# Performance work log

Measured on AMD Instinct MI355X. Metric: run time of the kernel, lower is better.

Reference implementation:

```python
import jax, jax.numpy as jnp
import numpy as np

STRIDE = 16
H = 100
W = 100
C = 1024
A = 9  # anchors per location
IOU_THRESH = 0.7
MIN_SIZE = 16.0


def _conv2d(x, w, b):
    # x: [N,C,H,W], w: [O,I,kh,kw] (torch OIHW), 'same' padding, stride 1
    y = jax.lax.conv_general_dilated(
        x, w, window_strides=(1, 1), padding='SAME',
        dimension_numbers=('NCHW', 'OIHW', 'NCHW'))
    return y + b[None, :, None, None]


def _nms_keep(boxes, valid, iou_thresh):
    # boxes: [N,4] (y1,x1,y2,x2) sorted by descending score; valid: [N] bool
    n = boxes.shape[0]
    y1, x1, y2, x2 = boxes[:, 0], boxes[:, 1], boxes[:, 2], boxes[:, 3]
    areas = (y2 - y1) * (x2 - x1)
    idx = jnp.arange(n)

    def body(i, keep):
        iy1 = jnp.maximum(y1[i], y1)
        ix1 = jnp.maximum(x1[i], x1)
        iy2 = jnp.minimum(y2[i], y2)
        ix2 = jnp.minimum(x2[i], x2)
        inter = jnp.maximum(iy2 - iy1, 0.0) * jnp.maximum(ix2 - ix1, 0.0)
        iou = inter / (areas[i] + areas - inter + 1e-8)
        suppress = (iou > iou_thresh) & (idx > i)
        return jnp.where(keep[i], keep & ~suppress, keep)

    return jax.lax.fori_loop(0, n, body, valid)


def _make_anchor_map():
    ratios = np.array([0.5, 1.0, 2.0])
    sizes = np.array([128.0, 256.0, 512.0])
    ah = (sizes[:, None] * np.sqrt(ratios)[None, :]).reshape(-1)  # [9]
    aw = (sizes[:, None] / np.sqrt(ratios)[None, :]).reshape(-1)  # [9]
    cy = (np.arange(H) + 0.5) * STRIDE
    cx = (np.arange(W) + 0.5) * STRIDE
    am = np.zeros((H, W, A, 4), dtype=np.float32)
    am[..., 0] = cy[:, None, None]
    am[..., 1] = cx[None, :, None]
    am[..., 2] = ah[None, None, :]
    am[..., 3] = aw[None, None, :]
    return jnp.asarray(am.reshape(H, W, A * 4))


def setup_inputs() -> dict:
    key = jax.random.key(0)
    ks = jax.random.split(key, 4)
    feature_map = jax.random.normal(ks[0], (1, C, H, W), jnp.float32)
    # module init: normal(0, 0.01) weights, zero biases
    w1 = jax.random.normal(ks[1], (C, C, 3, 3), jnp.float32) * 0.01
    b1 = jnp.zeros((C,), jnp.float32)
    w_cls = jax.random.normal(ks[2], (A, C, 1, 1), jnp.float32) * 0.01
    b_cls = jnp.zeros((A,), jnp.float32)
    w_box = jax.random.normal(ks[3], (A * 4, C, 1, 1), jnp.float32) * 0.01
    b_box = jnp.zeros((A * 4,), jnp.float32)
    return {
        'feature_map': feature_map,
        'image_shape': jnp.array([3, H * STRIDE, W * STRIDE], jnp.int32),
        'anchor_map': _make_anchor_map(),
        'anchor_valid_map': jnp.ones((H, W, A), jnp.int32),
        'max_proposals_pre_nms': 6000,
        'max_proposals_post_nms': 300,
        'w1': w1, 'b1': b1,
        'w_cls': w_cls, 'b_cls': b_cls,
        'w_box': w_box, 'b_box': b_box,
    }


def reference(feature_map, image_shape, anchor_map, anchor_valid_map,
              max_proposals_pre_nms, max_proposals_post_nms,
              w1, b1, w_cls, b_cls, w_box, b_box):
    pre = int(max_proposals_pre_nms)
    post = int(max_proposals_post_nms)

    y = jax.nn.relu(_conv2d(feature_map, w1, b1))
    objectness_score_map = jax.nn.sigmoid(_conv2d(y, w_cls, b_cls))  # [1,9,H,W]
    box_deltas_map = _conv2d(y, w_box, b_box)                        # [1,36,H,W]
    # NCHW -> NHWC, like permute(0,2,3,1)
    objectness_score_map = jnp.transpose(objectness_score_map, (0, 2, 3, 1))
    box_deltas_map = jnp.transpose(box_deltas_map, (0, 2, 3, 1))

    h, w, a = anchor_valid_map.shape
    n = h * w * a
    anchors = anchor_map.reshape(n, 4)                # (cy, cx, ah, aw)
    scores = objectness_score_map.reshape(n)
    deltas = jax.lax.stop_gradient(box_deltas_map.reshape(n, 4))  # .detach()
    # allow_edge_proposals=True -> no valid filtering

    # decode (means=0, stds=1): center = c + t*s, size = s*exp(t)
    center = anchors[:, 0:2] + deltas[:, 0:2] * anchors[:, 2:4]
    size = anchors[:, 2:4] * jnp.exp(deltas[:, 2:4])
    proposals = jnp.concatenate([center - 0.5 * size, center + 0.5 * size], axis=1)

    # argsort ascending then flip == descending (matches torch code)
    order = jnp.argsort(scores)[::-1][:pre]
    proposals = proposals[order]
    scores_sorted = scores[order]

    # clip to image
    y1x1 = jnp.maximum(proposals[:, 0:2], 0.0)
    y2 = jnp.minimum(proposals[:, 2], image_shape[1].astype(proposals.dtype))
    x2 = jnp.minimum(proposals[:, 3], image_shape[2].astype(proposals.dtype))
    proposals = jnp.concatenate([y1x1, y2[:, None], x2[:, None]], axis=1)

    height = proposals[:, 2] - proposals[:, 0]
    width = proposals[:, 3] - proposals[:, 1]
    valid = (height >= MIN_SIZE) & (width >= MIN_SIZE)

    keep = _nms_keep(proposals, valid, IOU_THRESH)

    # fixed-shape selection of first `post` kept boxes (score-ordered)
    pos = jnp.where(keep, jnp.arange(pre), pre)
    pos = jnp.sort(pos)[:post]
    ok = pos < pre
    safe = jnp.minimum(pos, pre - 1)
    out_proposals = jnp.where(ok[:, None], proposals[safe], 0.0)  # [post,4]

    return objectness_score_map, box_deltas_map, out_proposals
```

## Files before the change

### kernel.cpp

```cpp
#include <hip/hip_runtime.h>
#include <hip/hip_fp16.h>
#include <stdint.h>

#define HH 100
#define WW 100
#define NPIX 10000
#define CIN 1024
#define COUT 1024
#define NA 9
#define NANCH 90000
#define PRE 6000
#define POST 300
#define SORTN 131072
#define MASKW 96
#define NW 94
#define K9 9216
#define SPAD 10404
#define WSCALE 1024.0f
#define KH 48

#define PXT 160
#define ABYTES 8192
#define BBYTES 10240
#define BUFB 36864
#define NSTEP 288

typedef unsigned short u16;
typedef _Float16 f16x8 __attribute__((ext_vector_type(8)));
typedef float f32x4 __attribute__((ext_vector_type(4)));

__device__ __forceinline__ void gload16(const u16* g, char* l)
{
    __builtin_amdgcn_global_load_lds((const void*)g, (void*)l, 16, 0, 0);
}

__global__ __launch_bounds__(256) void xsplit(
    const float* __restrict__ x, u16* __restrict__ xt1, u16* __restrict__ xt2)
{
    __shared__ unsigned sh[32][257];
    const int t = threadIdx.x;
    const int px0 = blockIdx.x * 32;
    const int ci0 = blockIdx.y * 256;
    for (int it = 0; it < 32; ++it) {
        int idx = it * 256 + t;
        int a = idx >> 5, b = idx & 31;
        int p = px0 + b;
        float v = (p < NPIX) ? x[(size_t)(ci0 + a) * NPIX + p] : 0.f;
        __half h1 = __float2half_rn(v);
        __half h2 = __float2half_rn(v - __half2float(h1));
        sh[b][a] = ((unsigned)__half_as_ushort(h1) << 16) | __half_as_ushort(h2);
    }
    __syncthreads();
    for (int it = 0; it < 8; ++it) {
        int u = it * 256 + t;
        int pl = u >> 6, cq = u & 63;
        int p = px0 + pl;
        if (p >= NPIX) continue;
        int r = p / 100, c = p - r * 100;
        int spx = (r + 1) * 102 + (c + 1);
        unsigned w0 = sh[pl][cq * 4 + 0], w1 = sh[pl][cq * 4 + 1];
        unsigned w2 = sh[pl][cq * 4 + 2], w3 = sh[pl][cq * 4 + 3];
        ushort4 v1 = make_ushort4((u16)(w0 >> 16), (u16)(w1 >> 16), (u16)(w2 >> 16), (u16)(w3 >> 16));
        ushort4 v2 = make_ushort4((u16)(w0 & 0xffff), (u16)(w1 & 0xffff), (u16)(w2 & 0xffff), (u16)(w3 & 0xffff));
        size_t o = (size_t)spx * 1024 + ci0 + cq * 4;
        *(ushort4*)&xt1[o] = v1;
        *(ushort4*)&xt2[o] = v2;
    }
}

__global__ __launch_bounds__(256) void xborder(u16* __restrict__ xt1, u16* __restrict__ xt2)
{
    const int idx = blockIdx.x;
    int spx;
    if (idx < 102) spx = idx;
    else if (idx < 204) spx = 10302 + (idx - 102);
    else { int k = idx - 204; spx = (1 + (k >> 1)) * 102 + (k & 1) * 101; }
    const int t = threadIdx.x;
    size_t o = (size_t)spx * 1024 + t * 4;
    *(ushort4*)&xt1[o] = make_ushort4(0, 0, 0, 0);
    *(ushort4*)&xt2[o] = make_ushort4(0, 0, 0, 0);
}

__global__ __launch_bounds__(256) void wsplit(
    const float* __restrict__ w1, u16* __restrict__ wp1, u16* __restrict__ wp2)
{
    __shared__ float sw[K9];
    const int t = threadIdx.x;
    const int co = blockIdx.x;
    for (int it = 0; it < 36; ++it)
        sw[it * 256 + t] = w1[(size_t)co * K9 + it * 256 + t];
    __syncthreads();
    for (int tap = 0; tap < 9; ++tap) {
        for (int it = 0; it < 4; ++it) {
            int ci = it * 256 + t;
            float v = sw[ci * 9 + tap] * WSCALE;
            __half h1 = __float2half_rn(v);
            __half h2 = __float2half_rn(v - __half2float(h1));
            size_t o = (size_t)tap * (COUT * 1024) + (size_t)co * 1024 + ci;
            wp1[o] = __half_as_ushort(h1);
            wp2[o] = __half_as_ushort(h2);
        }
    }
}

__global__ __launch_bounds__(256, 2) void conv_mfma(
    const u16* __restrict__ xt1, const u16* __restrict__ xt2,
    const u16* __restrict__ wp1, const u16* __restrict__ wp2,
    const float* __restrict__ b1, float* __restrict__ y)
{
    __shared__ __align__(16) char lds[2 * BUFB];
    const int t = threadIdx.x;
    const int co0 = blockIdx.x * 128;
    const int px0 = blockIdx.y * PXT;
    const int lane = t & 63;
    const int wv = __builtin_amdgcn_readfirstlane(t >> 6);
    const int wm = (wv >> 1) * 64;
    const int wn = (wv & 1) * 80;

    const int qs = (lane & 3) ^ ((lane >> 3) & 3);
    const int aln = (lane >> 2) * 1024 + qs * 8;

    const int ar0 = wv * 32, ar1 = wv * 32 + 16;
    const size_t aOff0 = (size_t)(co0 + ar0) * 1024 + aln;
    const size_t aOff1 = (size_t)(co0 + ar1) * 1024 + aln;

    const int nb = (wv < 2) ? 3 : 2;
    size_t bOff[3]; int bLds[3];
#pragma unroll
    for (int s = 0; s < 3; ++s) {
        int r0 = (wv + 4 * s) * 16;
        if (r0 >= PXT) r0 = 0;
        int p = px0 + r0 + (lane >> 2);
        if (p > NPIX - 1) p = NPIX - 1;
        int rr = p / 100, cc = p - rr * 100;
        bOff[s] = (size_t)((rr + 1) * 102 + cc + 1) * 1024 + qs * 8;
        bLds[s] = r0 * 64;
    }

    const int qf = ((lane >> 4) ^ (((lane & 15) >> 1) & 3)) * 16;
    const int fA = (wm + (lane & 15)) * 64 + qf;
    const int fB = 16384 + (wn + (lane & 15)) * 64 + qf;

    f32x4 acc[4][5] = {};

    auto STAGE = [&](int buf, int tap, int ci0) {
        const int dy = (tap * 11) >> 5;
        const int tsh = (dy - 1) * 102 + (tap - dy * 3) - 1;
        const size_t adelta = (size_t)tap * 1048576 + ci0;
        const ptrdiff_t bdelta = (ptrdiff_t)tsh * 1024 + ci0;
        char* lb = lds + buf * BUFB;
        gload16(wp1 + aOff0 + adelta, lb + ar0 * 64);
        gload16(wp1 + aOff1 + adelta, lb + ar1 * 64);
        gload16(wp2 + aOff0 + adelta, lb + ABYTES + ar0 * 64);
        gload16(wp2 + aOff1 + adelta, lb + ABYTES + ar1 * 64);
#pragma unroll
        for (int s = 0; s < 3; ++s) {
            if (s < nb) {
                gload16(xt1 + (ptrdiff_t)bOff[s] + bdelta, lb + 16384 + bLds[s]);
                gload16(xt2 + (ptrdiff_t)bOff[s] + bdelta, lb + 26624 + bLds[s]);
            }
        }
    };

    auto COMPUTE = [&](int buf) {
        const char* lb = lds + buf * BUFB;
        f16x8 A1[4], A2[4], B1[5], B2[5];
#pragma unroll
        for (int mi = 0; mi < 4; ++mi) {
            A1[mi] = *(const f16x8*)(lb + fA + mi * 1024);
            A2[mi] = *(const f16x8*)(lb + ABYTES + fA + mi * 1024);
        }
#pragma unroll
        for (int ni = 0; ni < 5; ++ni) {
            B1[ni] = *(const f16x8*)(lb + fB + ni * 1024);
            B2[ni] = *(const f16x8*)(lb + BBYTES + fB + ni * 1024);
        }
#pragma unroll
        for (int mi = 0; mi < 4; ++mi)
#pragma unroll
            for (int ni = 0; ni < 5; ++ni) {
                acc[mi][ni] = __builtin_amdgcn_mfma_f32_16x16x32_f16(A1[mi], B1[ni], acc[mi][ni], 0, 0, 0);
                acc[mi][ni] = __builtin_amdgcn_mfma_f32_16x16x32_f16(A1[mi], B2[ni], acc[mi][ni], 0, 0, 0);
                acc[mi][ni] = __builtin_amdgcn_mfma_f32_16x16x32_f16(A2[mi], B1[ni], acc[mi][ni], 0, 0, 0);
            }
    };

    STAGE(0, 0, 0);
    __syncthreads();
    for (int kk = 0; kk < NSTEP - 1; ++kk) {
        const int kn = kk + 1;
        STAGE(kn & 1, kn >> 5, (kn & 31) << 5);
        COMPUTE(kk & 1);
        __syncthreads();
    }
    COMPUTE((NSTEP - 1) & 1);

    const int q4 = (lane >> 4) * 4, nl = lane & 15;
    const float inv = 1.0f / WSCALE;
#pragma unroll
    for (int mi = 0; mi < 4; ++mi) {
        const int cob = co0 + wm + mi * 16 + q4;
        const float bb0 = b1[cob + 0], bb1 = b1[cob + 1];
        const float bb2 = b1[cob + 2], bb3 = b1[cob + 3];
#pragma unroll
        for (int ni = 0; ni < 5; ++ni) {
            const int px = px0 + wn + ni * 16 + nl;
            if (px < NPIX) {
                y[(size_t)(cob + 0) * NPIX + px] = fmaxf(acc[mi][ni][0] * inv + bb0, 0.f);
                y[(size_t)(cob + 1) * NPIX + px] = fmaxf(acc[mi][ni][1] * inv + bb1, 0.f);
                y[(size_t)(cob + 2) * NPIX + px] = fmaxf(acc[mi][ni][2] * inv + bb2, 0.f);
                y[(size_t)(cob + 3) * NPIX + px] = fmaxf(acc[mi][ni][3] * inv + bb3, 0.f);
            }
        }
    }
}

__global__ __launch_bounds__(256) void wh_prep(
    const float* __restrict__ wcls, const float* __restrict__ wbox,
    float* __restrict__ wh)
{
    int e = blockIdx.x * 256 + threadIdx.x;
    if (e >= CIN * KH) return;
    int c = e / KH, k = e - c * KH;
    float v = 0.f;
    if (k < 9) v = wcls[k * CIN + c];
    else if (k < 45) v = wbox[(k - 9) * CIN + c];
    wh[e] = v;
}

__global__ __launch_bounds__(256) void rpn_head(
    const float* __restrict__ y, const float* __restrict__ wh,
    const float* __restrict__ bcls, const float* __restrict__ bbox,
    const float* __restrict__ am, const int* __restrict__ ishape,
    float* __restrict__ out_scores, float* __restrict__ out_deltas,
    float4* __restrict__ boxes, unsigned long long* __restrict__ keys)
{
    __shared__ float red[4][64][KH + 1];
    const int t = threadIdx.x;
    const int lane = t & 63;
    const int q = __builtin_amdgcn_readfirstlane(t >> 6);
    const int p = blockIdx.x * 64 + lane;
    const int pp = (p < NPIX) ? p : (NPIX - 1);

    float acc[45];
#pragma unroll
    for (int k = 0; k < 45; ++k) acc[k] = 0.f;

    const float* __restrict__ yq  = y  + (size_t)q * 256 * NPIX + pp;
    const float* __restrict__ whq = wh + (size_t)q * 256 * KH;
    for (int c = 0; c < 256; ++c) {
        float yv = yq[(size_t)c * NPIX];
        const float* wr = whq + c * KH;
#pragma unroll
        for (int k = 0; k < 45; ++k) acc[k] += yv * wr[k];
    }

#pragma unroll
    for (int k = 0; k < 45; ++k) red[q][lane][k] = acc[k];
    __syncthreads();

    if (t >= 64 || p >= NPIX) return;

    float s[45];
#pragma unroll
    for (int k = 0; k < 45; ++k)
        s[k] = (red[0][lane][k] + red[1][lane][k]) + (red[2][lane][k] + red[3][lane][k]);

    const float imh = (float)ishape[1], imw = (float)ishape[2];
#pragma unroll
    for (int a = 0; a < 9; ++a) {
        const int i = p * NA + a;
        float logit = s[a] + bcls[a];
        float score = 1.f / (1.f + expf(-logit));
        float d0 = s[9 + a * 4 + 0] + bbox[a * 4 + 0];
        float d1 = s[9 + a * 4 + 1] + bbox[a * 4 + 1];
        float d2 = s[9 + a * 4 + 2] + bbox[a * 4 + 2];
        float d3 = s[9 + a * 4 + 3] + bbox[a * 4 + 3];
        out_scores[i] = score;
        out_deltas[i * 4 + 0] = d0;
        out_deltas[i * 4 + 1] = d1;
        out_deltas[i * 4 + 2] = d2;
        out_deltas[i * 4 + 3] = d3;

        float cy = am[i * 4 + 0], cx = am[i * 4 + 1];
        float ah = am[i * 4 + 2], aw = am[i * 4 + 3];
        float ctry = cy + d0 * ah, ctrx = cx + d1 * aw;
        float hh = ah * expf(d2), ww = aw * expf(d3);
        float y1 = fmaxf(ctry - 0.5f * hh, 0.f);
        float x1 = fmaxf(ctrx - 0.5f * ww, 0.f);
        float y2 = fminf(ctry + 0.5f * hh, imh);
        float x2 = fminf(ctrx + 0.5f * ww, imw);
        boxes[i] = make_float4(y1, x1, y2, x2);
        unsigned sb = __float_as_uint(score);
        keys[i] = ((unsigned long long)sb << 32) | (unsigned)i;
    }
}

__global__ __launch_bounds__(256) void key_pad(unsigned long long* __restrict__ keys)
{
    int i = NANCH + blockIdx.x * 256 + threadIdx.x;
    if (i < SORTN) keys[i] = 0ull;
}

__global__ __launch_bounds__(256) void bitonic_local(unsigned long long* keys)
{
    __shared__ unsigned long long s[2048];
    const int base = blockIdx.x * 2048, t = threadIdx.x;
    for (int k = t; k < 2048; k += 256) s[k] = keys[base + k];
    for (int L = 2; L <= 2048; L <<= 1) {
        for (int d = L >> 1; d >= 1; d >>= 1) {
            __syncthreads();
            for (int pr = t; pr < 1024; pr += 256) {
                int i = ((pr & ~(d - 1)) << 1) | (pr & (d - 1));
                int j = i + d;
                bool desc = (((base + i) & L) == 0);
                unsigned long long va = s[i], vb = s[j];
                bool sw = desc ? (va < vb) : (va > vb);
                if (sw) { s[i] = vb; s[j] = va; }
            }
        }
    }
    __syncthreads();
    for (int k = t; k < 2048; k += 256) keys[base + k] = s[k];
}

__global__ __launch_bounds__(256) void bitonic_gpass(unsigned long long* keys, int L, int d)
{
    int pr = blockIdx.x * 256 + threadIdx.x;
    int i = ((pr & ~(d - 1)) << 1) | (pr & (d - 1));
    int j = i + d;
    bool desc = ((i & L) == 0);
    unsigned long long va = keys[i], vb = keys[j];
    bool sw = desc ? (va < vb) : (va > vb);
    if (sw) { keys[i] = vb; keys[j] = va; }
}

__global__ __launch_bounds__(256) void bitonic_lmerge(unsigned long long* keys, int L)
{
    __shared__ unsigned long long s[2048];
    const int base = blockIdx.x * 2048, t = threadIdx.x;
    for (int k = t; k < 2048; k += 256) s[k] = keys[base + k];
    const bool desc = ((base & L) == 0);
    for (int d = 1024; d >= 1; d >>= 1) {
        __syncthreads();
        for (int pr = t; pr < 1024; pr += 256) {
            int i = ((pr & ~(d - 1)) << 1) | (pr & (d - 1));
            int j = i + d;
            unsigned long long va = s[i], vb = s[j];
            bool sw = desc ? (va < vb) : (va > vb);
            if (sw) { s[i] = vb; s[j] = va; }
        }
    }
    __syncthreads();
    for (int k = t; k < 2048; k += 256) keys[base + k] = s[k];
}

__global__ __launch_bounds__(256) void gather_sorted(
    const unsigned long long* __restrict__ keys, const float4* __restrict__ boxes,
    float4* __restrict__ box_s, unsigned long long* __restrict__ validw)
{
    int s = blockIdx.x * 256 + threadIdx.x;
    bool valid = false;
    if (s < PRE) {
        unsigned idx = (unsigned)(keys[s] & 0xffffffffull);
        float4 b = boxes[idx];
        box_s[s] = b;
        valid = ((b.z - b.x) >= 16.f) && ((b.w - b.y) >= 16.f);
    }
    unsigned long long bal = __ballot(valid);
    if ((threadIdx.x & 63) == 0) validw[s >> 6] = bal;
}

__global__ __launch_bounds__(128) void nms_mask(
    const float4* __restrict__ box_s, unsigned long long* __restrict__ mask)
{
    const int i = blockIdx.x;
    const int w = threadIdx.x;
    if (w >= NW) return;
    float4 bi = box_s[i];
    float areai = (bi.z - bi.x) * (bi.w - bi.y);
    unsigned long long m = 0ull;
    const int j0 = w * 64;
    if (j0 + 63 > i) {
#pragma unroll 4
        for (int b = 0; b < 64; ++b) {
            int j = j0 + b;
            if (j <= i || j >= PRE) continue;
            float4 bj = box_s[j];
            float areaj = (bj.z - bj.x) * (bj.w - bj.y);
            float iy1 = fmaxf(bi.x, bj.x), ix1 = fmaxf(bi.y, bj.y);
            float iy2 = fminf(bi.z, bj.z), ix2 = fminf(bi.w, bj.w);
            float inter = fmaxf(iy2 - iy1, 0.f) * fmaxf(ix2 - ix1, 0.f);
            float iou = inter / (areai + areaj - inter + 1e-8f);
            if (iou > 0.7f) m |= (1ull << b);
        }
    }
    mask[(size_t)i * MASKW + w] = m;
}

__global__ __launch_bounds__(64) void nms_scan(
    const unsigned long long* __restrict__ mask,
    const unsigned long long* __restrict__ validw,
    unsigned long long* __restrict__ keepw)
{
    const int l = threadIdx.x;
    unsigned long long r0 = ~validw[l];
    unsigned long long r1 = (l < NW - 64) ? ~validw[64 + l] : ~0ull;

    unsigned long long p0[16], p1[16];
#pragma unroll
    for (int k = 0; k < 16; ++k) {
        p0[k] = mask[(size_t)k * MASKW + l];
        p1[k] = (l < NW - 64) ? mask[(size_t)k * MASKW + 64 + l] : 0ull;
    }
    int kept = 0;
    for (int w = 0; w < NW && kept < POST; ++w) {
        unsigned long long Wc = (w < 64) ? __shfl(r0, w) : __shfl(r1, w - 64);
#pragma unroll 16
        for (int b = 0; b < 64; ++b) {
            int i = w * 64 + b;
            if (i >= PRE) break;
            int slot = i & 15;
            unsigned long long m0 = p0[slot], m1 = p1[slot];
            int nxt = i + 16;
            if (nxt < PRE) {
                p0[slot] = mask[(size_t)nxt * MASKW + l];
                p1[slot] = (l < NW - 64) ? mask[(size_t)nxt * MASKW + 64 + l] : 0ull;
            }
            if (!((Wc >> b) & 1ull)) {
                r0 |= m0; r1 |= m1;
                Wc = (w < 64) ? __shfl(r0, w) : __shfl(r1, w - 64);
                ++kept;
            }
        }
    }
    keepw[l] = ~r0;
    if (l < NW - 64) keepw[64 + l] = ~r1;
}

__global__ __launch_bounds__(256) void out_gather(
    const unsigned long long* __restrict__ keepw,
    const float4* __restrict__ box_s, float* __restrict__ outp)
{
    __shared__ unsigned long long kw_s[NW];
    __shared__ int prefix[NW];
    const int t = threadIdx.x;
    if (t < NW) kw_s[t] = keepw[t];
    __syncthreads();
    if (t == 0) {
        int cum = 0;
        for (int w = 0; w < NW; ++w) { prefix[w] = cum; cum += __popcll(kw_s[w]); }
    }
    for (int k = t; k < POST * 4; k += 256) outp[k] = 0.f;
    __syncthreads();
    for (int i = t; i < PRE; i += 256) {
        int w = i >> 6, b = i & 63;
        unsigned long long kw = kw_s[w];
        if ((kw >> b) & 1ull) {
            int rank = prefix[w] + __popcll(kw & ((1ull << b) - 1ull));
            if (rank < POST) {
                float4 bx = box_s[i];
                outp[rank * 4 + 0] = bx.x;
                outp[rank * 4 + 1] = bx.y;
                outp[rank * 4 + 2] = bx.z;
                outp[rank * 4 + 3] = bx.w;
            }
        }
    }
}

extern "C" void kernel_launch(void* const* d_in, const int* in_sizes, int n_in,
                              void* d_out, int out_size, void* d_ws, size_t ws_size,
                              hipStream_t stream)
{
    const float* x      = (const float*)d_in[0];
    const int*   ishape = (const int*)  d_in[1];
    const float* am     = (const float*)d_in[2];
    const float* w1   = (const float*)d_in[6];
    const float* b1   = (const float*)d_in[7];
    const float* wcls = (const float*)d_in[8];
    const float* bcls = (const float*)d_in[9];
    const float* wbox = (const float*)d_in[10];
    const float* bbox = (const float*)d_in[11];
    float* out = (float*)d_out;

    char* ws = (char*)d_ws;
    size_t off = 0;
    float* y  = (float*)(ws + off);  off += (size_t)COUT * NPIX * 4;
    u16* xt1  = (u16*)(ws + off);    off += (size_t)SPAD * 1024 * 2;
    u16* xt2  = (u16*)(ws + off);    off += (size_t)SPAD * 1024 * 2;
    u16* wp1  = (u16*)(ws + off);    off += (size_t)9 * COUT * 1024 * 2;
    u16* wp2  = (u16*)(ws + off);    off += (size_t)9 * COUT * 1024 * 2;
    float4* boxes = (float4*)(ws + off);              off += (size_t)NANCH * 16;
    unsigned long long* keys = (unsigned long long*)(ws + off); off += (size_t)SORTN * 8;
    float4* box_s = (float4*)(ws + off);              off += (size_t)PRE * 16;
    unsigned long long* validw = (unsigned long long*)(ws + off); off += 96 * 8;
    unsigned long long* keepw  = (unsigned long long*)(ws + off); off += 96 * 8;
    unsigned long long* maskb  = (unsigned long long*)(ws + off); off += (size_t)PRE * MASKW * 8;
    float* wh = (float*)(ws + off);  off += (size_t)CIN * KH * 4;

    xsplit<<<dim3(313, 4), 256, 0, stream>>>(x, xt1, xt2);
    xborder<<<404, 256, 0, stream>>>(xt1, xt2);
    wsplit<<<COUT, 256, 0, stream>>>(w1, wp1, wp2);
    wh_prep<<<(CIN * KH + 255) / 256, 256, 0, stream>>>(wcls, wbox, wh);
    conv_mfma<<<dim3(8, (NPIX + PXT - 1) / PXT), 256, 0, stream>>>(xt1, xt2, wp1, wp2, b1, y);
    rpn_head<<<(NPIX + 63) / 64, 256, 0, stream>>>(y, wh, bcls, bbox, am, ishape,
                                                   out, out + NANCH, boxes, keys);
    key_pad<<<(SORTN - NANCH + 255) / 256, 256, 0, stream>>>(keys);
    bitonic_local<<<SORTN / 2048, 256, 0, stream>>>(keys);
    for (int L = 4096; L <= SORTN; L <<= 1) {
        for (int d = L >> 1; d >= 2048; d >>= 1)
            bitonic_gpass<<<SORTN / 512, 256, 0, stream>>>(keys, L, d);
        bitonic_lmerge<<<SORTN / 2048, 256, 0, stream>>>(keys, L);
    }
    gather_sorted<<<24, 256, 0, stream>>>(keys, boxes, box_s, validw);
    nms_mask<<<PRE, 128, 0, stream>>>(box_s, maskb);
    nms_scan<<<1, 64, 0, stream>>>(maskb, validw, keepw);
    out_gather<<<1, 256, 0, stream>>>(keepw, box_s, out + (size_t)NANCH * 5);
}
```

Baseline: 1.138 ms.

## Replace full bitonic sort with histogram top-k selection and small sort

Swaps the full 131072-element multi-launch bitonic sort for a selection: a 16-bit histogram of the score bits, a threshold search for the top PRE bucket, atomic compaction of candidates, then a single-block bitonic sort of at most 8192 keys in shared memory fused with the box gather. This cuts the many global sort passes and kernel launches. The risk is that if more than 8192 keys land at or above the threshold bucket (heavy ties), candidates get dropped. Compaction order is also nondeterministic, though the final sort restores the order.

```diff
diff --git a/kernel.cpp b/kernel.cpp
--- a/kernel.cpp
+++ b/kernel.cpp
@@ -11,13 +11,13 @@
 #define NANCH 90000
 #define PRE 6000
 #define POST 300
-#define SORTN 131072
 #define MASKW 96
 #define NW 94
 #define K9 9216
 #define SPAD 10404
 #define WSCALE 1024.0f
 #define KH 48
+#define CANDN 8192
 
 #define PXT 160
 #define ABYTES 8192
@@ -296,24 +296,77 @@
     }
 }
 
-__global__ __launch_bounds__(256) void key_pad(unsigned long long* __restrict__ keys)
-{
-    int i = NANCH + blockIdx.x * 256 + threadIdx.x;
-    if (i < SORTN) keys[i] = 0ull;
-}
-
-__global__ __launch_bounds__(256) void bitonic_local(unsigned long long* keys)
-{
-    __shared__ unsigned long long s[2048];
-    const int base = blockIdx.x * 2048, t = threadIdx.x;
-    for (int k = t; k < 2048; k += 256) s[k] = keys[base + k];
-    for (int L = 2; L <= 2048; L <<= 1) {
+__global__ __launch_bounds__(256) void score_hist(
+    const unsigned long long* __restrict__ keys, unsigned* __restrict__ hist)
+{
+    int i = blockIdx.x * 256 + threadIdx.x;
+    if (i < NANCH) atomicAdd(&hist[(unsigned)(keys[i] >> 48)], 1u);
+}
+
+__global__ __launch_bounds__(256) void score_thresh(
+    const unsigned* __restrict__ hist, unsigned* __restrict__ Pout)
+{
+    __shared__ unsigned csum[256];
+    __shared__ unsigned binv[256];
+    __shared__ int bc[2];
+    const int t = threadIdx.x;
+    unsigned sum = 0;
+    for (int i = 0; i < 256; ++i) sum += hist[t * 256 + i];
+    csum[t] = sum;
+    __syncthreads();
+    if (t == 0) {
+        unsigned cum = 0; int cstar = 0; unsigned cumPrev = 0;
+        for (int c = 255; c >= 0; --c) {
+            if (cum + csum[c] >= PRE) { cstar = c; cumPrev = cum; break; }
+            cum += csum[c];
+        }
+        bc[0] = cstar; bc[1] = (int)cumPrev;
+    }
+    __syncthreads();
+    const int cstar = bc[0];
+    binv[t] = hist[cstar * 256 + t];
+    __syncthreads();
+    if (t == 0) {
+        unsigned cum = (unsigned)bc[1];
+        unsigned P = (unsigned)cstar * 256;
+        for (int b = 255; b >= 0; --b) {
+            cum += binv[b];
+            if (cum >= PRE) { P = (unsigned)cstar * 256 + (unsigned)b; break; }
+        }
+        *Pout = P;
+    }
+}
+
+__global__ __launch_bounds__(256) void score_compact(
+    const unsigned long long* __restrict__ keys, const unsigned* __restrict__ Pout,
+    unsigned long long* __restrict__ cand, unsigned* __restrict__ cnt)
+{
+    int i = blockIdx.x * 256 + threadIdx.x;
+    if (i >= NANCH) return;
+    unsigned long long k = keys[i];
+    if ((unsigned)(k >> 48) >= *Pout) {
+        unsigned pos = atomicAdd(cnt, 1u);
+        if (pos < CANDN) cand[pos] = k;
+    }
+}
+
+__global__ __launch_bounds__(1024) void sort_gather(
+    const unsigned long long* __restrict__ cand, const unsigned* __restrict__ cnt,
+    const float4* __restrict__ boxes,
+    float4* __restrict__ box_s, unsigned long long* __restrict__ validw)
+{
+    __shared__ unsigned long long s[CANDN];
+    const int t = threadIdx.x;
+    int n = (int)*cnt; if (n > CANDN) n = CANDN;
+    for (int k = t; k < CANDN; k += 1024)
+        s[k] = (k < n) ? cand[k] : 0ull;
+    for (int L = 2; L <= CANDN; L <<= 1) {
         for (int d = L >> 1; d >= 1; d >>= 1) {
             __syncthreads();
-            for (int pr = t; pr < 1024; pr += 256) {
+            for (int pr = t; pr < CANDN / 2; pr += 1024) {
                 int i = ((pr & ~(d - 1)) << 1) | (pr & (d - 1));
                 int j = i + d;
-                bool desc = (((base + i) & L) == 0);
+                bool desc = ((i & L) == 0);
                 unsigned long long va = s[i], vb = s[j];
                 bool sw = desc ? (va < vb) : (va > vb);
                 if (sw) { s[i] = vb; s[j] = va; }
@@ -321,54 +374,14 @@
         }
     }
     __syncthreads();
-    for (int k = t; k < 2048; k += 256) keys[base + k] = s[k];
-}
-
-__global__ __launch_bounds__(256) void bitonic_gpass(unsigned long long* keys, int L, int d)
-{
-    int pr = blockIdx.x * 256 + threadIdx.x;
-    int i = ((pr & ~(d - 1)) << 1) | (pr & (d - 1));
-    int j = i + d;
-    bool desc = ((i & L) == 0);
-    unsigned long long va = keys[i], vb = keys[j];
-    bool sw = desc ? (va < vb) : (va > vb);
-    if (sw) { keys[i] = vb; keys[j] = va; }
-}
-
-__global__ __launch_bounds__(256) void bitonic_lmerge(unsigned long long* keys, int L)
-{
-    __shared__ unsigned long long s[2048];
-    const int base = blockIdx.x * 2048, t = threadIdx.x;
-    for (int k = t; k < 2048; k += 256) s[k] = keys[base + k];
-    const bool desc = ((base & L) == 0);
-    for (int d = 1024; d >= 1; d >>= 1) {
-        __syncthreads();
-        for (int pr = t; pr < 1024; pr += 256) {
-            int i = ((pr & ~(d - 1)) << 1) | (pr & (d - 1));
-            int j = i + d;
-            unsigned long long va = s[i], vb = s[j];
-            bool sw = desc ? (va < vb) : (va > vb);
-            if (sw) { s[i] = vb; s[j] = va; }
-        }
-    }
-    __syncthreads();
-    for (int k = t; k < 2048; k += 256) keys[base + k] = s[k];
-}
-
-__global__ __launch_bounds__(256) void gather_sorted(
-    const unsigned long long* __restrict__ keys, const float4* __restrict__ boxes,
-    float4* __restrict__ box_s, unsigned long long* __restrict__ validw)
-{
-    int s = blockIdx.x * 256 + threadIdx.x;
-    bool valid = false;
-    if (s < PRE) {
-        unsigned idx = (unsigned)(keys[s] & 0xffffffffull);
+    for (int k = t; k < PRE; k += 1024) {
+        unsigned idx = (unsigned)(s[k] & 0xffffffffull);
         float4 b = boxes[idx];
-        box_s[s] = b;
-        valid = ((b.z - b.x) >= 16.f) && ((b.w - b.y) >= 16.f);
-    }
-    unsigned long long bal = __ballot(valid);
-    if ((threadIdx.x & 63) == 0) validw[s >> 6] = bal;
+        box_s[k] = b;
+        bool valid = ((b.z - b.x) >= 16.f) && ((b.w - b.y) >= 16.f);
+        unsigned long long bal = __ballot(valid);
+        if ((t & 63) == 0) validw[k >> 6] = bal;
+    }
 }
 
 __global__ __launch_bounds__(128) void nms_mask(
@@ -492,12 +505,18 @@
     u16* wp1  = (u16*)(ws + off);    off += (size_t)9 * COUT * 1024 * 2;
     u16* wp2  = (u16*)(ws + off);    off += (size_t)9 * COUT * 1024 * 2;
     float4* boxes = (float4*)(ws + off);              off += (size_t)NANCH * 16;
-    unsigned long long* keys = (unsigned long long*)(ws + off); off += (size_t)SORTN * 8;
+    unsigned long long* keys = (unsigned long long*)(ws + off); off += (size_t)NANCH * 8;
     float4* box_s = (float4*)(ws + off);              off += (size_t)PRE * 16;
     unsigned long long* validw = (unsigned long long*)(ws + off); off += 96 * 8;
     unsigned long long* keepw  = (unsigned long long*)(ws + off); off += 96 * 8;
     unsigned long long* maskb  = (unsigned long long*)(ws + off); off += (size_t)PRE * MASKW * 8;
     float* wh = (float*)(ws + off);  off += (size_t)CIN * KH * 4;
+    unsigned* hist = (unsigned*)(ws + off); off += 65536 * 4;
+    unsigned long long* cand = (unsigned long long*)(ws + off); off += (size_t)CANDN * 8;
+    unsigned* cntP = (unsigned*)(ws + off); off += 64;
+
+    hipMemsetAsync(hist, 0, 65536 * 4, stream);
+    hipMemsetAsync(cntP, 0, 64, stream);
 
     xsplit<<<dim3(313, 4), 256, 0, stream>>>(x, xt1, xt2);
     xborder<<<404, 256, 0, stream>>>(xt1, xt2);
@@ -506,14 +525,10 @@
     conv_mfma<<<dim3(8, (NPIX + PXT - 1) / PXT), 256, 0, stream>>>(xt1, xt2, wp1, wp2, b1, y);
     rpn_head<<<(NPIX + 63) / 64, 256, 0, stream>>>(y, wh, bcls, bbox, am, ishape,
                                                    out, out + NANCH, boxes, keys);
-    key_pad<<<(SORTN - NANCH + 255) / 256, 256, 0, stream>>>(keys);
-    bitonic_local<<<SORTN / 2048, 256, 0, stream>>>(keys);
-    for (int L = 4096; L <= SORTN; L <<= 1) {
-        for (int d = L >> 1; d >= 2048; d >>= 1)
-            bitonic_gpass<<<SORTN / 512, 256, 0, stream>>>(keys, L, d);
-        bitonic_lmerge<<<SORTN / 2048, 256, 0, stream>>>(keys, L);
-    }
-    gather_sorted<<<24, 256, 0, stream>>>(keys, boxes, box_s, validw);
+    score_hist<<<(NANCH + 255) / 256, 256, 0, stream>>>(keys, hist);
+    score_thresh<<<1, 256, 0, stream>>>(hist, cntP + 1);
+    score_compact<<<(NANCH + 255) / 256, 256, 0, stream>>>(keys, cntP + 1, cand, cntP);
+    sort_gather<<<1, 1024, 0, stream>>>(cand, cntP, boxes, box_s, validw);
     nms_mask<<<PRE, 128, 0, stream>>>(box_s, maskb);
     nms_scan<<<1, 64, 0, stream>>>(maskb, validw, keepw);
     out_gather<<<1, 256, 0, stream>>>(keepw, box_s, out + (size_t)NANCH * 5);
```

New measurement: 1.263 ms. 11.0% more time.

## Prefilter top scores via histogram threshold before bitonic sort

Applied to the files above, without the earlier changes.

Builds a 65536-bin histogram on the top 16 bits of each score key inside the head kernel. A single-block kernel uses it to find a bin threshold that keeps at least PRE candidates. Keys at or above that threshold are compacted with an atomic counter into an 8192-entry buffer. Only that buffer is bitonic-sorted, replacing the full 131072-element padded sort and its many launches. The cost is extra atomics, three memsets and two small kernels. Candidates past 8192, possible if many scores share the threshold bin, are silently dropped.

```diff
diff --git a/kernel.cpp b/kernel.cpp
--- a/kernel.cpp
+++ b/kernel.cpp
@@ -11,13 +11,13 @@
 #define NANCH 90000
 #define PRE 6000
 #define POST 300
-#define SORTN 131072
 #define MASKW 96
 #define NW 94
 #define K9 9216
 #define SPAD 10404
 #define WSCALE 1024.0f
 #define KH 48
+#define CANDN 8192
 
 #define PXT 160
 #define ABYTES 8192
@@ -233,7 +233,8 @@
     const float* __restrict__ bcls, const float* __restrict__ bbox,
     const float* __restrict__ am, const int* __restrict__ ishape,
     float* __restrict__ out_scores, float* __restrict__ out_deltas,
-    float4* __restrict__ boxes, unsigned long long* __restrict__ keys)
+    float4* __restrict__ boxes, unsigned long long* __restrict__ keys,
+    unsigned* __restrict__ hist)
 {
     __shared__ float red[4][64][KH + 1];
     const int t = threadIdx.x;
@@ -293,13 +294,55 @@
         boxes[i] = make_float4(y1, x1, y2, x2);
         unsigned sb = __float_as_uint(score);
         keys[i] = ((unsigned long long)sb << 32) | (unsigned)i;
-    }
-}
-
-__global__ __launch_bounds__(256) void key_pad(unsigned long long* __restrict__ keys)
-{
-    int i = NANCH + blockIdx.x * 256 + threadIdx.x;
-    if (i < SORTN) keys[i] = 0ull;
+        atomicAdd(&hist[sb >> 16], 1u);
+    }
+}
+
+__global__ __launch_bounds__(256) void score_thresh(
+    const unsigned* __restrict__ hist, unsigned* __restrict__ Pout)
+{
+    __shared__ unsigned csum[256];
+    __shared__ unsigned binv[256];
+    __shared__ int bc[2];
+    const int t = threadIdx.x;
+    unsigned sum = 0;
+    for (int i = 0; i < 256; ++i) sum += hist[t * 256 + i];
+    csum[t] = sum;
+    __syncthreads();
+    if (t == 0) {
+        unsigned cum = 0; int cstar = 0; unsigned cumPrev = 0;
+        for (int c = 255; c >= 0; --c) {
+            if (cum + csum[c] >= PRE) { cstar = c; cumPrev = cum; break; }
+            cum += csum[c];
+        }
+        bc[0] = cstar; bc[1] = (int)cumPrev;
+    }
+    __syncthreads();
+    const int cstar = bc[0];
+    binv[t] = hist[cstar * 256 + t];
+    __syncthreads();
+    if (t == 0) {
+        unsigned cum = (unsigned)bc[1];
+        unsigned P = (unsigned)cstar * 256;
+        for (int b = 255; b >= 0; --b) {
+            cum += binv[b];
+            if (cum >= PRE) { P = (unsigned)cstar * 256 + (unsigned)b; break; }
+        }
+        *Pout = P;
+    }
+}
+
+__global__ __launch_bounds__(256) void score_compact(
+    const unsigned long long* __restrict__ keys, const unsigned* __restrict__ Pout,
+    unsigned long long* __restrict__ cand, unsigned* __restrict__ cnt)
+{
+    int i = blockIdx.x * 256 + threadIdx.x;
+    if (i >= NANCH) return;
+    unsigned long long k = keys[i];
+    if ((unsigned)(k >> 48) >= *Pout) {
+        unsigned pos = atomicAdd(cnt, 1u);
+        if (pos < CANDN) cand[pos] = k;
+    }
 }
 
 __global__ __launch_bounds__(256) void bitonic_local(unsigned long long* keys)
@@ -492,12 +535,19 @@
     u16* wp1  = (u16*)(ws + off);    off += (size_t)9 * COUT * 1024 * 2;
     u16* wp2  = (u16*)(ws + off);    off += (size_t)9 * COUT * 1024 * 2;
     float4* boxes = (float4*)(ws + off);              off += (size_t)NANCH * 16;
-    unsigned long long* keys = (unsigned long long*)(ws + off); off += (size_t)SORTN * 8;
+    unsigned long long* keys = (unsigned long long*)(ws + off); off += (size_t)NANCH * 8;
     float4* box_s = (float4*)(ws + off);              off += (size_t)PRE * 16;
     unsigned long long* validw = (unsigned long long*)(ws + off); off += 96 * 8;
     unsigned long long* keepw  = (unsigned long long*)(ws + off); off += 96 * 8;
     unsigned long long* maskb  = (unsigned long long*)(ws + off); off += (size_t)PRE * MASKW * 8;
     float* wh = (float*)(ws + off);  off += (size_t)CIN * KH * 4;
+    unsigned* hist = (unsigned*)(ws + off); off += 65536 * 4;
+    unsigned long long* cand = (unsigned long long*)(ws + off); off += (size_t)CANDN * 8;
+    unsigned* cntP = (unsigned*)(ws + off); off += 64;
+
+    hipMemsetAsync(hist, 0, 65536 * 4, stream);
+    hipMemsetAsync(cand, 0, (size_t)CANDN * 8, stream);
+    hipMemsetAsync(cntP, 0, 64, stream);
 
     xsplit<<<dim3(313, 4), 256, 0, stream>>>(x, xt1, xt2);
     xborder<<<404, 256, 0, stream>>>(xt1, xt2);
@@ -505,15 +555,16 @@
     wh_prep<<<(CIN * KH + 255) / 256, 256, 0, stream>>>(wcls, wbox, wh);
     conv_mfma<<<dim3(8, (NPIX + PXT - 1) / PXT), 256, 0, stream>>>(xt1, xt2, wp1, wp2, b1, y);
     rpn_head<<<(NPIX + 63) / 64, 256, 0, stream>>>(y, wh, bcls, bbox, am, ishape,
-                                                   out, out + NANCH, boxes, keys);
-    key_pad<<<(SORTN - NANCH + 255) / 256, 256, 0, stream>>>(keys);
-    bitonic_local<<<SORTN / 2048, 256, 0, stream>>>(keys);
-    for (int L = 4096; L <= SORTN; L <<= 1) {
+                                                   out, out + NANCH, boxes, keys, hist);
+    score_thresh<<<1, 256, 0, stream>>>(hist, cntP + 1);
+    score_compact<<<(NANCH + 255) / 256, 256, 0, stream>>>(keys, cntP + 1, cand, cntP);
+    bitonic_local<<<CANDN / 2048, 256, 0, stream>>>(cand);
+    for (int L = 4096; L <= CANDN; L <<= 1) {
         for (int d = L >> 1; d >= 2048; d >>= 1)
-            bitonic_gpass<<<SORTN / 512, 256, 0, stream>>>(keys, L, d);
-        bitonic_lmerge<<<SORTN / 2048, 256, 0, stream>>>(keys, L);
-    }
-    gather_sorted<<<24, 256, 0, stream>>>(keys, boxes, box_s, validw);
+            bitonic_gpass<<<CANDN / 512, 256, 0, stream>>>(cand, L, d);
+        bitonic_lmerge<<<CANDN / 2048, 256, 0, stream>>>(cand, L);
+    }
+    gather_sorted<<<24, 256, 0, stream>>>(cand, boxes, box_s, validw);
     nms_mask<<<PRE, 128, 0, stream>>>(box_s, maskb);
     nms_scan<<<1, 64, 0, stream>>>(maskb, validw, keepw);
     out_gather<<<1, 256, 0, stream>>>(keepw, box_s, out + (size_t)NANCH * 5);
```

New measurement: 1.249 ms. 1.1x slower.

## Load conv weight fragments directly to registers in MFMA-ready layout, skipping LDS

Applied to the files above, without the earlier changes.

The weight-split kernel now writes the two fp16 weight halves in a fragment-ordered layout, so each lane can read its MFMA A operand straight from global memory with one 16-byte load. The conv kernel drops the A tiles from LDS, which shrinks the per-buffer LDS footprint, and double-buffers the A fragments in registers, loading them one step ahead of the compute. This removes LDS traffic and round trips for the weights. In exchange it adds register pressure and puts global-load latency directly on the MFMA operands, with weights no longer shared through LDS between the waves that reuse them.

```diff
diff --git a/kernel.cpp b/kernel.cpp
--- a/kernel.cpp
+++ b/kernel.cpp
@@ -20,9 +20,8 @@
 #define KH 48
 
 #define PXT 160
-#define ABYTES 8192
 #define BBYTES 10240
-#define BUFB 36864
+#define BUFB 20480
 #define NSTEP 288
 
 typedef unsigned short u16;
@@ -82,30 +81,41 @@
 }
 
 __global__ __launch_bounds__(256) void wsplit(
-    const float* __restrict__ w1, u16* __restrict__ wp1, u16* __restrict__ wp2)
+    const float* __restrict__ w1, u16* __restrict__ wpf1, u16* __restrict__ wpf2)
 {
     __shared__ float sw[K9];
     const int t = threadIdx.x;
     const int co = blockIdx.x;
+    const int m = co >> 4, r = co & 15;
     for (int it = 0; it < 36; ++it)
         sw[it * 256 + t] = w1[(size_t)co * K9 + it * 256 + t];
     __syncthreads();
-    for (int tap = 0; tap < 9; ++tap) {
-        for (int it = 0; it < 4; ++it) {
-            int ci = it * 256 + t;
-            float v = sw[ci * 9 + tap] * WSCALE;
+    for (int it = 0; it < 5; ++it) {
+        int idx = it * 256 + t;
+        if (idx >= 1152) break;
+        int tap = idx >> 7, oct = idx & 127;
+        int g = oct >> 2, chunk = oct & 3;
+        int ci0 = oct * 8;
+        u16 h1v[8], h2v[8];
+#pragma unroll
+        for (int j = 0; j < 8; ++j) {
+            float v = sw[(ci0 + j) * 9 + tap] * WSCALE;
             __half h1 = __float2half_rn(v);
             __half h2 = __float2half_rn(v - __half2float(h1));
-            size_t o = (size_t)tap * (COUT * 1024) + (size_t)co * 1024 + ci;
-            wp1[o] = __half_as_ushort(h1);
-            wp2[o] = __half_as_ushort(h2);
-        }
+            h1v[j] = __half_as_ushort(h1);
+            h2v[j] = __half_as_ushort(h2);
+        }
+        size_t o = ((size_t)((tap * 32 + g) * 64) + m) * 512 + (size_t)(r + chunk * 16) * 8;
+        *(ushort4*)&wpf1[o]     = make_ushort4(h1v[0], h1v[1], h1v[2], h1v[3]);
+        *(ushort4*)&wpf1[o + 4] = make_ushort4(h1v[4], h1v[5], h1v[6], h1v[7]);
+        *(ushort4*)&wpf2[o]     = make_ushort4(h2v[0], h2v[1], h2v[2], h2v[3]);
+        *(ushort4*)&wpf2[o + 4] = make_ushort4(h2v[4], h2v[5], h2v[6], h2v[7]);
     }
 }
 
 __global__ __launch_bounds__(256, 2) void conv_mfma(
     const u16* __restrict__ xt1, const u16* __restrict__ xt2,
-    const u16* __restrict__ wp1, const u16* __restrict__ wp2,
+    const u16* __restrict__ wpf1, const u16* __restrict__ wpf2,
     const float* __restrict__ b1, float* __restrict__ y)
 {
     __shared__ __align__(16) char lds[2 * BUFB];
@@ -116,13 +126,9 @@
     const int wv = __builtin_amdgcn_readfirstlane(t >> 6);
     const int wm = (wv >> 1) * 64;
     const int wn = (wv & 1) * 80;
+    const int cog = (co0 >> 4) + (wm >> 4);
 
     const int qs = (lane & 3) ^ ((lane >> 3) & 3);
-    const int aln = (lane >> 2) * 1024 + qs * 8;
-
-    const int ar0 = wv * 32, ar1 = wv * 32 + 16;
-    const size_t aOff0 = (size_t)(co0 + ar0) * 1024 + aln;
-    const size_t aOff1 = (size_t)(co0 + ar1) * 1024 + aln;
 
     const int nb = (wv < 2) ? 3 : 2;
     size_t bOff[3]; int bLds[3];
@@ -138,38 +144,39 @@
     }
 
     const int qf = ((lane >> 4) ^ (((lane & 15) >> 1) & 3)) * 16;
-    const int fA = (wm + (lane & 15)) * 64 + qf;
-    const int fB = 16384 + (wn + (lane & 15)) * 64 + qf;
+    const int fB = (wn + (lane & 15)) * 64 + qf;
 
     f32x4 acc[4][5] = {};
-
-    auto STAGE = [&](int buf, int tap, int ci0) {
+    f16x8 A1a[4], A2a[4], A1b[4], A2b[4];
+
+    auto STAGE = [&](int buf, int step) {
+        const int tap = step >> 5;
+        const int ci0 = (step & 31) << 5;
         const int dy = (tap * 11) >> 5;
         const int tsh = (dy - 1) * 102 + (tap - dy * 3) - 1;
-        const size_t adelta = (size_t)tap * 1048576 + ci0;
         const ptrdiff_t bdelta = (ptrdiff_t)tsh * 1024 + ci0;
         char* lb = lds + buf * BUFB;
-        gload16(wp1 + aOff0 + adelta, lb + ar0 * 64);
-        gload16(wp1 + aOff1 + adelta, lb + ar1 * 64);
-        gload16(wp2 + aOff0 + adelta, lb + ABYTES + ar0 * 64);
-        gload16(wp2 + aOff1 + adelta, lb + ABYTES + ar1 * 64);
 #pragma unroll
         for (int s = 0; s < 3; ++s) {
             if (s < nb) {
-                gload16(xt1 + (ptrdiff_t)bOff[s] + bdelta, lb + 16384 + bLds[s]);
-                gload16(xt2 + (ptrdiff_t)bOff[s] + bdelta, lb + 26624 + bLds[s]);
+                gload16(xt1 + (ptrdiff_t)bOff[s] + bdelta, lb + bLds[s]);
+                gload16(xt2 + (ptrdiff_t)bOff[s] + bdelta, lb + BBYTES + bLds[s]);
             }
         }
     };
 
-    auto COMPUTE = [&](int buf) {
+    auto LOADA = [&](f16x8* D1, f16x8* D2, int sp) {
+        const size_t ab = ((size_t)sp * 64 + cog) * 512 + (size_t)(lane * 8);
+#pragma unroll
+        for (int mi = 0; mi < 4; ++mi) {
+            D1[mi] = *(const f16x8*)(wpf1 + ab + mi * 512);
+            D2[mi] = *(const f16x8*)(wpf2 + ab + mi * 512);
+        }
+    };
+
+    auto COMPUTE = [&](int buf, const f16x8* A1, const f16x8* A2) {
         const char* lb = lds + buf * BUFB;
-        f16x8 A1[4], A2[4], B1[5], B2[5];
-#pragma unroll
-        for (int mi = 0; mi < 4; ++mi) {
-            A1[mi] = *(const f16x8*)(lb + fA + mi * 1024);
-            A2[mi] = *(const f16x8*)(lb + ABYTES + fA + mi * 1024);
-        }
+        f16x8 B1[5], B2[5];
 #pragma unroll
         for (int ni = 0; ni < 5; ++ni) {
             B1[ni] = *(const f16x8*)(lb + fB + ni * 1024);
@@ -185,15 +192,19 @@
             }
     };
 
-    STAGE(0, 0, 0);
-    __syncthreads();
-    for (int kk = 0; kk < NSTEP - 1; ++kk) {
-        const int kn = kk + 1;
-        STAGE(kn & 1, kn >> 5, (kn & 31) << 5);
-        COMPUTE(kk & 1);
+    STAGE(0, 0);
+    LOADA(A1a, A2a, 0);
+    __syncthreads();
+    for (int kk = 0; kk < NSTEP; kk += 2) {
+        if (kk + 1 < NSTEP) STAGE(1, kk + 1);
+        LOADA(A1b, A2b, (kk + 1 < NSTEP) ? kk + 1 : NSTEP - 1);
+        COMPUTE(0, A1a, A2a);
         __syncthreads();
-    }
-    COMPUTE((NSTEP - 1) & 1);
+        if (kk + 2 < NSTEP) STAGE(0, kk + 2);
+        LOADA(A1a, A2a, (kk + 2 < NSTEP) ? kk + 2 : NSTEP - 1);
+        COMPUTE(1, A1b, A2b);
+        __syncthreads();
+    }
 
     const int q4 = (lane >> 4) * 4, nl = lane & 15;
     const float inv = 1.0f / WSCALE;
@@ -489,8 +500,8 @@
     float* y  = (float*)(ws + off);  off += (size_t)COUT * NPIX * 4;
     u16* xt1  = (u16*)(ws + off);    off += (size_t)SPAD * 1024 * 2;
     u16* xt2  = (u16*)(ws + off);    off += (size_t)SPAD * 1024 * 2;
-    u16* wp1  = (u16*)(ws + off);    off += (size_t)9 * COUT * 1024 * 2;
-    u16* wp2  = (u16*)(ws + off);    off += (size_t)9 * COUT * 1024 * 2;
+    u16* wpf1 = (u16*)(ws + off);    off += (size_t)9 * COUT * 1024 * 2;
+    u16* wpf2 = (u16*)(ws + off);    off += (size_t)9 * COUT * 1024 * 2;
     float4* boxes = (float4*)(ws + off);              off += (size_t)NANCH * 16;
     unsigned long long* keys = (unsigned long long*)(ws + off); off += (size_t)SORTN * 8;
     float4* box_s = (float4*)(ws + off);              off += (size_t)PRE * 16;
@@ -501,9 +512,9 @@
 
     xsplit<<<dim3(313, 4), 256, 0, stream>>>(x, xt1, xt2);
     xborder<<<404, 256, 0, stream>>>(xt1, xt2);
-    wsplit<<<COUT, 256, 0, stream>>>(w1, wp1, wp2);
+    wsplit<<<COUT, 256, 0, stream>>>(w1, wpf1, wpf2);
     wh_prep<<<(CIN * KH + 255) / 256, 256, 0, stream>>>(wcls, wbox, wh);
-    conv_mfma<<<dim3(8, (NPIX + PXT - 1) / PXT), 256, 0, stream>>>(xt1, xt2, wp1, wp2, b1, y);
+    conv_mfma<<<dim3(8, (NPIX + PXT - 1) / PXT), 256, 0, stream>>>(xt1, xt2, wpf1, wpf2, b1, y);
     rpn_head<<<(NPIX + 63) / 64, 256, 0, stream>>>(y, wh, bcls, bbox, am, ishape,
                                                    out, out + NANCH, boxes, keys);
     key_pad<<<(SORTN - NANCH + 255) / 256, 256, 0, stream>>>(keys);
```

Result: slower. 1.178 ms (+3.5%).
